# Optimization experiments

Hardware: AMD Instinct MI355X
Metric: run time of the kernel (lower is better)

Reference implementation:

```python
import jax, jax.numpy as jnp
import numpy as np

HIDDEN = 1024
GMM = 16


def setup_inputs() -> dict:
    key = jax.random.key(0)
    ks = jax.random.split(key, 9)
    B, T, D, S = 16, 1024, HIDDEN, 512
    sc_ih = 1.0 / np.sqrt(2 * D)
    sc_hh = 1.0 / np.sqrt(D)
    return {
        "input_h_c": jax.random.normal(ks[0], (B, T, D), jnp.float32),
        "memory": jax.random.normal(ks[1], (B, S, D), jnp.float32),
        "input_lengths": jax.random.randint(ks[2], (B,), 1, S + 1),
        "W_ih": jax.random.uniform(ks[3], (4 * D, 2 * D), jnp.float32, -sc_ih, sc_ih),
        "W_hh": jax.random.uniform(ks[4], (4 * D, D), jnp.float32, -sc_hh, sc_hh),
        "b_ih": jax.random.uniform(ks[5], (4 * D,), jnp.float32, -sc_hh, sc_hh),
        "b_hh": jax.random.uniform(ks[6], (4 * D,), jnp.float32, -sc_hh, sc_hh),
        "Wg_w": jax.random.uniform(ks[7], (3 * GMM, D), jnp.float32, -sc_hh, sc_hh),
        "Wg_b": jax.random.uniform(ks[8], (3 * GMM,), jnp.float32, -sc_hh, sc_hh),
    }


def reference(input_h_c, memory, input_lengths, W_ih, W_hh, b_ih, b_hh, Wg_w, Wg_b):
    B, T, D = input_h_c.shape
    S = memory.shape[1]
    M = Wg_b.shape[0] // 3
    b = b_ih + b_hh
    u = jnp.arange(S, dtype=input_h_c.dtype)  # positions u

    def step(carry, x_t):
        h, c, ctx = carry
        x = jnp.concatenate([x_t, ctx], axis=-1)  # [B, 2D]
        gates = x @ W_ih.T + h @ W_hh.T + b  # [B, 4D], torch gate order i,f,g,o
        i_g, f_g, g_g, o_g = jnp.split(gates, 4, axis=-1)
        c = jax.nn.sigmoid(f_g) * c + jax.nn.sigmoid(i_g) * jnp.tanh(g_g)
        h = jax.nn.sigmoid(o_g) * jnp.tanh(c)
        phi = h @ Wg_w.T + Wg_b  # [B, 3M]
        ksi = jnp.exp(phi[:, :M])
        beta = jnp.exp(phi[:, M:2 * M])
        alpha = jax.nn.softmax(phi[:, 2 * M:], axis=-1)
        # 1/(1+exp((ksi-u)/beta)) == sigmoid((u-ksi)/beta)
        z = (u[None, None, :] - ksi[:, :, None]) / beta[:, :, None]  # [B,M,S]
        half = 0.5 / beta[:, :, None]
        F_R = jax.nn.sigmoid(z + half)  # CDF at u+0.5
        F_L = jax.nn.sigmoid(z - half)  # CDF at u-0.5
        w = jnp.einsum('bm,bms->bs', alpha, F_R - F_L)  # [B,S]
        term = 1.0 - jnp.einsum('bm,bms->bs', alpha, F_R)  # [B,S]
        ctx = jnp.einsum('bs,bsd->bd', w, memory)  # [B,D]
        return (h, c, ctx), (w, term)

    h0 = jnp.zeros((B, D), input_h_c.dtype)
    c0 = jnp.zeros((B, D), input_h_c.dtype)
    ctx0 = jnp.zeros((B, D), input_h_c.dtype)
    (h, c, ctx), (ws, terms) = jax.lax.scan(
        step, (h0, c0, ctx0), jnp.swapaxes(input_h_c, 0, 1))
    alignment = jnp.swapaxes(ws, 0, 1)  # [B,T,S]
    term_last = terms[-1]  # [B,S]
    termination = jnp.take_along_axis(term_last, (input_lengths - 1)[:, None], axis=1)  # [B,1]
    context = ctx[:, None, :]  # [B,1,D], last-step context (as returned by torch forward)
    return (context, alignment, termination)
```

## Files before the change

kernel.cpp:

```cpp
#include <hip/hip_runtime.h>
#include <hip/hip_fp16.h>

#define BB 16
#define TT 1024
#define DD 1024
#define SS 512
#define KK2 2048

#define NBLK 128
#define NTHR 512

#define OUT_ALIGN 16384
#define OUT_TERM  8404992

typedef __attribute__((ext_vector_type(8))) short short8;
typedef __attribute__((ext_vector_type(4))) float floatx4;
typedef __attribute__((ext_vector_type(2))) _Float16 half2v;

struct KParams {
  const float* x;
  const float* mem;
  const int*   lens;
  const float* W_ih;
  const float* W_hh;
  const float* b_ih;
  const float* b_hh;
  const float* Wg_w;
  const float* Wg_b;
  float* out;
  unsigned* bar;
  unsigned short* xc0;
  unsigned short* xc1;
  unsigned* wgbf;
};

__device__ __forceinline__ float sigf(float v) {
  return __builtin_amdgcn_rcpf(1.0f + __expf(-v));
}
__device__ __forceinline__ float tanhfast(float v) {
  float a = fabsf(v);
  float e = __expf(-2.0f * a);
  float r = (1.0f - e) * __builtin_amdgcn_rcpf(1.0f + e);
  return v < 0.0f ? -r : r;
}

__device__ __forceinline__ unsigned short f2bf(float f) {
  unsigned u = __float_as_uint(f);
  return (unsigned short)((u + 0x7FFFu + ((u >> 16) & 1u)) >> 16);
}
__device__ __forceinline__ float bf2f(unsigned short h) {
  return __uint_as_float(((unsigned)h) << 16);
}
__device__ __forceinline__ unsigned pack2bf(float a, float b) {
  return (unsigned)f2bf(a) | ((unsigned)f2bf(b) << 16);
}
__device__ __forceinline__ unsigned cvtpk(float a, float b) {
  unsigned r;
  asm volatile("v_cvt_pk_bf16_f32 %0, %1, %2" : "=v"(r) : "v"(a), "v"(b));
  return r;
}

__device__ __forceinline__ void cstore_u32(unsigned* p2, unsigned v) {
  __hip_atomic_store(p2, v, __ATOMIC_RELAXED, __HIP_MEMORY_SCOPE_AGENT);
}
__device__ __forceinline__ unsigned cload_u32(const unsigned* p2) {
  return __hip_atomic_load(p2, __ATOMIC_RELAXED, __HIP_MEMORY_SCOPE_AGENT);
}
__device__ __forceinline__ unsigned long long cload_u64(const unsigned long long* p2) {
  return __hip_atomic_load(p2, __ATOMIC_RELAXED, __HIP_MEMORY_SCOPE_AGENT);
}

__device__ __forceinline__ void lds_barrier() {
  asm volatile("s_waitcnt lgkmcnt(0)\n\ts_barrier" ::: "memory");
}

__device__ __forceinline__ void grid_barrier(unsigned* bar, unsigned ep, int blk) {
  __syncthreads();
  if (threadIdx.x == 0) cstore_u32(&bar[64 + blk * 32], ep);
  if (threadIdx.x < 64) {
    while (cload_u32(&bar[64 + (int)threadIdx.x * 32]) < ep) __builtin_amdgcn_s_sleep(1);
    while (cload_u32(&bar[64 + ((int)threadIdx.x + 64) * 32]) < ep) __builtin_amdgcn_s_sleep(1);
  }
  __syncthreads();
}

union UF { unsigned w[4]; unsigned long long u[2]; short8 s; };

#define MFMA16 __builtin_amdgcn_mfma_f32_16x16x32_bf16

__device__ __forceinline__ void xh_mfma(const UF* xf, const UF* hf, const short8* bfr,
                                        floatx4& a00, floatx4& a01,
                                        floatx4& a10, floatx4& a11) {
  floatx4 z = {0.f, 0.f, 0.f, 0.f};
  a00 = z; a01 = z; a10 = z; a11 = z;
  a00 = MFMA16(xf[0].s, bfr[0],  a00, 0, 0, 0); a01 = MFMA16(xf[1].s, bfr[1],  a01, 0, 0, 0);
  a10 = MFMA16(xf[0].s, bfr[12], a10, 0, 0, 0); a11 = MFMA16(xf[1].s, bfr[13], a11, 0, 0, 0);
  a00 = MFMA16(xf[2].s, bfr[2],  a00, 0, 0, 0); a01 = MFMA16(xf[3].s, bfr[3],  a01, 0, 0, 0);
  a10 = MFMA16(xf[2].s, bfr[14], a10, 0, 0, 0); a11 = MFMA16(xf[3].s, bfr[15], a11, 0, 0, 0);
  a00 = MFMA16(hf[0].s, bfr[8],  a00, 0, 0, 0); a01 = MFMA16(hf[1].s, bfr[9],  a01, 0, 0, 0);
  a10 = MFMA16(hf[0].s, bfr[20], a10, 0, 0, 0); a11 = MFMA16(hf[1].s, bfr[21], a11, 0, 0, 0);
  a00 = MFMA16(hf[2].s, bfr[10], a00, 0, 0, 0); a01 = MFMA16(hf[3].s, bfr[11], a01, 0, 0, 0);
  a10 = MFMA16(hf[2].s, bfr[22], a10, 0, 0, 0); a11 = MFMA16(hf[3].s, bfr[23], a11, 0, 0, 0);
}

__global__ __launch_bounds__(NTHR, 2) void tts_kernel(KParams p) {
  extern __shared__ char smem[];
  half2v* memsh2 = (half2v*)smem;

  __shared__ float redC[64 * 65 + 4];
  __shared__ unsigned hshu[8 * 65];
  __shared__ float php[384];
  __shared__ float alsh[16], ksish[16], invbsh[16];
  __shared__ float Rsh[513];
  __shared__ half2v wsh2[256];
  __shared__ float ctxp[4][128];
  __shared__ float bsh48[48];

  const int t    = threadIdx.x;
  const int blk  = blockIdx.x;
  const int lane = t & 63;
  const int w    = t >> 6;
  const int bbt  = blk & 15;
  const int dc   = blk >> 4;

  short8 bfr[24];
  {
    const int n = lane & 15;
    const int q = lane >> 4;
#pragma unroll
    for (int nt = 0; nt < 2; ++nt) {
      const int r = (n & 3) * 1024 + blk * 8 + nt * 4 + (n >> 2);
#pragma unroll
      for (int ki = 0; ki < 12; ++ki) {
        short8 v;
        const int k0 = (ki >> 2) * 1024 + w * 128 + (ki & 3) * 32 + q * 8;
#pragma unroll
        for (int j = 0; j < 8; ++j) {
          int k = k0 + j;
          float wv = (k < 2048) ? p.W_ih[(size_t)r * 2048 + k]
                                : p.W_hh[(size_t)r * 1024 + (k - 2048)];
          v[j] = (short)f2bf(wv);
        }
        bfr[nt * 12 + ki] = v;
      }
    }
  }
  float biasreg[4] = {0.f, 0.f, 0.f, 0.f};
  if (t < 128) {
    int dl = t & 7;
#pragma unroll
    for (int g = 0; g < 4; ++g) {
      int r = g * 1024 + blk * 8 + dl;
      biasreg[g] = p.b_ih[r] + p.b_hh[r];
    }
  }
  if (t < 48) bsh48[t] = p.Wg_b[t];
  {
    int dl = t & 127, sp = t >> 7;
    for (int pr = sp; pr < 256; pr += 4) {
      const float* mp = p.mem + (size_t)bbt * SS * DD + (size_t)(2 * pr) * DD + dc * 128 + dl;
      half2v v;
      v.x = (_Float16)mp[0];
      v.y = (_Float16)mp[DD];
      memsh2[pr * 128 + dl] = v;
    }
  }
  if (blk == 0) {
    for (int i = t; i < 48 * 512; i += NTHR)
      cstore_u32(&p.wgbf[i], pack2bf(p.Wg_w[2 * i], p.Wg_w[2 * i + 1]));
  }
  grid_barrier(p.bar, 1u, blk);

  float c_val = 0.0f;
  unsigned ep = 1;
  unsigned short* xc_cur = p.xc0;
  unsigned short* xc_nxt = p.xc1;
  const int ab2 = ((lane & 15) * KK2 + w * 128 + ((lane >> 4) * 8)) >> 2;
  const float* xrow = p.x + (size_t)(lane & 15) * TT * DD + w * 128 + ((lane >> 4) * 8);

  floatx4 acc00, acc01, acc10, acc11;
  {
    UF xf[4], hf[4];
#pragma unroll
    for (int sub = 0; sub < 4; ++sub) {
      floatx4 lo = *(const floatx4*)(xrow + sub * 32);
      floatx4 hi = *(const floatx4*)(xrow + sub * 32 + 4);
      xf[sub].w[0] = cvtpk(lo[0], lo[1]); xf[sub].w[1] = cvtpk(lo[2], lo[3]);
      xf[sub].w[2] = cvtpk(hi[0], hi[1]); xf[sub].w[3] = cvtpk(hi[2], hi[3]);
    }
    const unsigned long long* hb = (const unsigned long long*)p.xc0 + ab2 + 256;
#pragma unroll
    for (int sub = 0; sub < 4; ++sub) {
      hf[sub].u[0] = cload_u64(hb + sub * 8);
      hf[sub].u[1] = cload_u64(hb + sub * 8 + 1);
    }
    xh_mfma(xf, hf, bfr, acc00, acc01, acc10, acc11);
  }

  for (int tstep = 0; tstep < TT; ++tstep) {
    {
      const unsigned long long* cb = (const unsigned long long*)xc_cur + ab2;
      UF fc[4];
#pragma unroll
      for (int sub = 0; sub < 4; ++sub) {
        fc[sub].u[0] = cload_u64(cb + sub * 8);
        fc[sub].u[1] = cload_u64(cb + sub * 8 + 1);
      }
      floatx4 c00 = acc00, c01 = acc01, c10 = acc10, c11 = acc11;
      c00 = MFMA16(fc[0].s, bfr[4],  c00, 0, 0, 0); c01 = MFMA16(fc[1].s, bfr[5],  c01, 0, 0, 0);
      c10 = MFMA16(fc[0].s, bfr[16], c10, 0, 0, 0); c11 = MFMA16(fc[1].s, bfr[17], c11, 0, 0, 0);
      c00 = MFMA16(fc[2].s, bfr[6],  c00, 0, 0, 0); c01 = MFMA16(fc[3].s, bfr[7],  c01, 0, 0, 0);
      c10 = MFMA16(fc[2].s, bfr[18], c10, 0, 0, 0); c11 = MFMA16(fc[3].s, bfr[19], c11, 0, 0, 0);
      c00 += c01; c10 += c11;
#pragma unroll
      for (int reg = 0; reg < 4; ++reg) {
        redC[(w * 8 + reg) * 65 + lane]     = c00[reg];
        redC[(w * 8 + 4 + reg) * 65 + lane] = c10[reg];
      }
    }
    lds_barrier();
    if (t < 128) {
      int b = t >> 3, dl = t & 7, nt = dl >> 2, dl4 = dl & 3;
      int row = nt * 4 + (b & 3);
      float gate[4];
#pragma unroll
      for (int g = 0; g < 4; ++g) {
        int ls = ((b >> 2) << 4) | (dl4 * 4 + g);
        float s = biasreg[g];
#pragma unroll
        for (int w2 = 0; w2 < 8; ++w2) s += redC[(w2 * 8 + row) * 65 + ls];
        gate[g] = s;
      }
      c_val = sigf(gate[1]) * c_val + sigf(gate[0]) * tanhfast(gate[2]);
      float hv = sigf(gate[3]) * tanhfast(c_val);
      float hn = __shfl_down(hv, 1, 64);
      if ((t & 1) == 0)
        cstore_u32((unsigned*)(xc_nxt + b * KK2 + 1024 + blk * 8 + dl), pack2bf(hv, hn));
    }
    grid_barrier(p.bar, ++ep, blk);

    unsigned long long hword = 0;
    if (t < 256) hword = cload_u64((const unsigned long long*)xc_nxt + bbt * 512 + 256 + t);
    UF hf[4];
    floatx4 xlo[4], xhi[4];
    if (tstep + 1 < TT) {
      const unsigned long long* hb = (const unsigned long long*)xc_nxt + ab2 + 256;
#pragma unroll
      for (int sub = 0; sub < 4; ++sub) {
        hf[sub].u[0] = cload_u64(hb + sub * 8);
        hf[sub].u[1] = cload_u64(hb + sub * 8 + 1);
      }
      const float* xp = xrow + (size_t)(tstep + 1) * DD;
#pragma unroll
      for (int sub = 0; sub < 4; ++sub) {
        xlo[sub] = *(const floatx4*)(xp + sub * 32);
        xhi[sub] = *(const floatx4*)(xp + sub * 32 + 4);
      }
    }
    if (t < 256) {
      int row = t >> 5, col = (t & 31) * 2;
      hshu[row * 65 + col]     = (unsigned)hword;
      hshu[row * 65 + col + 1] = (unsigned)(hword >> 32);
    }
    lds_barrier();
    if (t < 384) {
      int m = t >> 3, part = t & 7;
      const unsigned* wgp = p.wgbf + m * 512 + part * 64;
      const unsigned* hrow = hshu + part * 65;
      float s0 = 0.f, s1 = 0.f, s2 = 0.f, s3 = 0.f;
#pragma unroll 4
      for (int i = 0; i < 64; i += 4) {
        unsigned u0 = hrow[i],     g0 = wgp[i];
        unsigned u1 = hrow[i + 1], g1 = wgp[i + 1];
        unsigned u2 = hrow[i + 2], g2 = wgp[i + 2];
        unsigned u3 = hrow[i + 3], g3 = wgp[i + 3];
        s0 += bf2f((unsigned short)u0) * bf2f((unsigned short)g0)
            + bf2f((unsigned short)(u0 >> 16)) * bf2f((unsigned short)(g0 >> 16));
        s1 += bf2f((unsigned short)u1) * bf2f((unsigned short)g1)
            + bf2f((unsigned short)(u1 >> 16)) * bf2f((unsigned short)(g1 >> 16));
        s2 += bf2f((unsigned short)u2) * bf2f((unsigned short)g2)
            + bf2f((unsigned short)(u2 >> 16)) * bf2f((unsigned short)(g2 >> 16));
        s3 += bf2f((unsigned short)u3) * bf2f((unsigned short)g3)
            + bf2f((unsigned short)(u3 >> 16)) * bf2f((unsigned short)(g3 >> 16));
      }
      php[t] = (s0 + s1) + (s2 + s3);
    }
    lds_barrier();
    if (t < 64) {
      float s = 0.f;
      if (t < 48) {
        s = bsh48[t];
#pragma unroll
        for (int i = 0; i < 8; ++i) s += php[t * 8 + i];
      }
      float mx = s;
#pragma unroll
      for (int o = 1; o < 16; o <<= 1) mx = fmaxf(mx, __shfl_xor(mx, o, 64));
      float e = __expf(s - mx);
      float sm = e;
#pragma unroll
      for (int o = 1; o < 16; o <<= 1) sm += __shfl_xor(sm, o, 64);
      float alpha_v = e * __builtin_amdgcn_rcpf(sm);
      float ksi_v   = __expf(s);
      float invb_v  = __expf(-s);
      if (t >= 32) { if (t < 48) alsh[t - 32] = alpha_v; }
      else if (t < 16) ksish[t] = ksi_v;
      else invbsh[t - 16] = invb_v;
      int m = t & 15;
      float am = __shfl(alpha_v, 32 + m, 64);
      float km = __shfl(ksi_v, m, 64);
      float bm = __shfl(invb_v, 16 + m, 64);
      float term = am * sigf((-0.5f - km) * bm);
#pragma unroll
      for (int o = 1; o < 16; o <<= 1) term += __shfl_xor(term, o, 64);
      if (t == 48) Rsh[0] = term;
    }
    lds_barrier();
    {
      float su = (float)t;
      float rv0 = 0.f, rv1 = 0.f;
#pragma unroll
      for (int m = 0; m < 16; m += 2) {
        rv0 += alsh[m]     * sigf((su + 0.5f - ksish[m])     * invbsh[m]);
        rv1 += alsh[m + 1] * sigf((su + 0.5f - ksish[m + 1]) * invbsh[m + 1]);
      }
      float rv = rv0 + rv1;
      float rvp = __shfl_up(rv, 1, 64);
      float rvn = __shfl_down(rv, 1, 64);
      Rsh[t + 1] = rv;
      if ((t & 1) == 0) {
        half2v v2;
        v2.x = (_Float16)(rv - rvp);
        v2.y = (_Float16)(rvn - rv);
        wsh2[t >> 1] = v2;
      }
      if (dc == 0 && (t & 63) != 0)
        p.out[OUT_ALIGN + ((size_t)bbt * TT + tstep) * SS + t] = rv - rvp;
    }
    lds_barrier();
    {
      if (dc == 0 && t < 8)
        p.out[OUT_ALIGN + ((size_t)bbt * TT + tstep) * SS + 64 * t] =
            Rsh[64 * t + 1] - Rsh[64 * t];
      if (tstep == TT - 1 && dc == 0 && t == 0)
        p.out[OUT_TERM + bbt] = 1.0f - Rsh[p.lens[bbt]];
      int dl = t & 127, sp = t >> 7;
      const int pb = sp * 64;
      half2v wa = wsh2[pb];       wa.x = (_Float16)(Rsh[2 * pb + 1] - Rsh[2 * pb]);
      half2v wb = wsh2[pb + 32];  wb.x = (_Float16)(Rsh[2 * pb + 65] - Rsh[2 * pb + 64]);
      float s0 = __builtin_amdgcn_fdot2(memsh2[pb * 128 + dl], wa, 0.f, false);
      float s1 = __builtin_amdgcn_fdot2(memsh2[(pb + 32) * 128 + dl], wb, 0.f, false);
#pragma unroll 8
      for (int q = 1; q < 32; ++q) {
        s0 = __builtin_amdgcn_fdot2(memsh2[(pb + q) * 128 + dl],      wsh2[pb + q],      s0, false);
        s1 = __builtin_amdgcn_fdot2(memsh2[(pb + 32 + q) * 128 + dl], wsh2[pb + 32 + q], s1, false);
      }
      ctxp[sp][dl] = s0 + s1;
    }
    lds_barrier();
    if (t < 128) {
      float cv = ctxp[0][t] + ctxp[1][t] + ctxp[2][t] + ctxp[3][t];
      if (tstep == TT - 1) p.out[bbt * DD + dc * 128 + t] = cv;
      float cvn = __shfl_down(cv, 1, 64);
      if ((t & 1) == 0)
        cstore_u32((unsigned*)(xc_nxt + bbt * KK2 + dc * 128 + t), pack2bf(cv, cvn));
    }
    __builtin_amdgcn_sched_barrier(0);
    if (tstep + 1 < TT) {
      UF xf[4];
#pragma unroll
      for (int sub = 0; sub < 4; ++sub) {
        xf[sub].w[0] = cvtpk(xlo[sub][0], xlo[sub][1]);
        xf[sub].w[1] = cvtpk(xlo[sub][2], xlo[sub][3]);
        xf[sub].w[2] = cvtpk(xhi[sub][0], xhi[sub][1]);
        xf[sub].w[3] = cvtpk(xhi[sub][2], xhi[sub][3]);
      }
      xh_mfma(xf, hf, bfr, acc00, acc01, acc10, acc11);
    }
    grid_barrier(p.bar, ++ep, blk);

    unsigned short* tmp = xc_cur; xc_cur = xc_nxt; xc_nxt = tmp;
  }
}

extern "C" void kernel_launch(void* const* d_in, const int* in_sizes, int n_in,
                              void* d_out, int out_size, void* d_ws, size_t ws_size,
                              hipStream_t stream) {
  (void)in_sizes; (void)n_in; (void)out_size; (void)ws_size;
  KParams p;
  p.x    = (const float*)d_in[0];
  p.mem  = (const float*)d_in[1];
  p.lens = (const int*)d_in[2];
  p.W_ih = (const float*)d_in[3];
  p.W_hh = (const float*)d_in[4];
  p.b_ih = (const float*)d_in[5];
  p.b_hh = (const float*)d_in[6];
  p.Wg_w = (const float*)d_in[7];
  p.Wg_b = (const float*)d_in[8];
  p.out  = (float*)d_out;
  p.bar  = (unsigned*)d_ws;
  p.xc0  = (unsigned short*)((char*)d_ws + 36864);
  p.xc1  = (unsigned short*)((char*)d_ws + 36864 + 65536);
  p.wgbf = (unsigned*)((char*)d_ws + 36864 + 131072);

  hipMemsetAsync(d_ws, 0, 36864 + 65536, stream);

  const unsigned dynLds = 131072;
  hipFuncSetAttribute((const void*)tts_kernel, hipFuncAttributeMaxDynamicSharedMemorySize,
                      (int)dynLds);

  void* args[] = { &p };
  hipLaunchCooperativeKernel((const void*)tts_kernel, dim3(NBLK), dim3(NTHR), args, dynLds,
                             stream);
}
```

Measured before the change: 16.19 ms.

## Compute attention phi projection with MFMA from register-resident Wg weights

Replaces the scalar bf16 dot-product phi projection (h @ Wg_w^T), which staged h through LDS and read a global bf16 copy of Wg, with MFMA instructions. These use Wg fragments preloaded into registers and the h fragments already loaded for the LSTM step. The setup grid barrier and global Wg staging are removed, and the grid barrier polling is simplified to one load per thread across 128 threads. The x-to-bf16 conversion is moved earlier. The aim is to shorten the serial per-timestep critical path, at the cost of 12 extra short8 registers per thread and redundant phi work across batch lanes.

```diff
diff --git a/kernel.cpp b/kernel.cpp
--- a/kernel.cpp
+++ b/kernel.cpp
@@ -31,7 +31,6 @@
   unsigned* bar;
   unsigned short* xc0;
   unsigned short* xc1;
-  unsigned* wgbf;
 };
 
 __device__ __forceinline__ float sigf(float v) {
@@ -48,9 +47,6 @@
   unsigned u = __float_as_uint(f);
   return (unsigned short)((u + 0x7FFFu + ((u >> 16) & 1u)) >> 16);
 }
-__device__ __forceinline__ float bf2f(unsigned short h) {
-  return __uint_as_float(((unsigned)h) << 16);
-}
 __device__ __forceinline__ unsigned pack2bf(float a, float b) {
   return (unsigned)f2bf(a) | ((unsigned)f2bf(b) << 16);
 }
@@ -77,9 +73,8 @@
 __device__ __forceinline__ void grid_barrier(unsigned* bar, unsigned ep, int blk) {
   __syncthreads();
   if (threadIdx.x == 0) cstore_u32(&bar[64 + blk * 32], ep);
-  if (threadIdx.x < 64) {
+  if (threadIdx.x < NBLK) {
     while (cload_u32(&bar[64 + (int)threadIdx.x * 32]) < ep) __builtin_amdgcn_s_sleep(1);
-    while (cload_u32(&bar[64 + ((int)threadIdx.x + 64) * 32]) < ep) __builtin_amdgcn_s_sleep(1);
   }
   __syncthreads();
 }
@@ -103,13 +98,16 @@
   a10 = MFMA16(hf[2].s, bfr[22], a10, 0, 0, 0); a11 = MFMA16(hf[3].s, bfr[23], a11, 0, 0, 0);
 }
 
+__device__ __forceinline__ float sel4(const floatx4& v, int r) {
+  return (r == 0) ? v[0] : (r == 1) ? v[1] : (r == 2) ? v[2] : v[3];
+}
+
 __global__ __launch_bounds__(NTHR, 2) void tts_kernel(KParams p) {
   extern __shared__ char smem[];
   half2v* memsh2 = (half2v*)smem;
 
   __shared__ float redC[64 * 65 + 4];
-  __shared__ unsigned hshu[8 * 65];
-  __shared__ float php[384];
+  __shared__ float phiP[384];
   __shared__ float alsh[16], ksish[16], invbsh[16];
   __shared__ float Rsh[513];
   __shared__ half2v wsh2[256];
@@ -144,6 +142,21 @@
         bfr[nt * 12 + ki] = v;
       }
     }
+  }
+  short8 wgB[12];
+  {
+    const int n = lane & 15;
+    const int q = lane >> 4;
+#pragma unroll
+    for (int tau = 0; tau < 3; ++tau)
+#pragma unroll
+      for (int c = 0; c < 4; ++c) {
+        short8 v;
+        const float* wg = p.Wg_w + (size_t)(tau * 16 + n) * 1024 + w * 128 + c * 32 + q * 8;
+#pragma unroll
+        for (int j = 0; j < 8; ++j) v[j] = (short)f2bf(wg[j]);
+        wgB[tau * 4 + c] = v;
+      }
   }
   float biasreg[4] = {0.f, 0.f, 0.f, 0.f};
   if (t < 128) {
@@ -165,14 +178,9 @@
       memsh2[pr * 128 + dl] = v;
     }
   }
-  if (blk == 0) {
-    for (int i = t; i < 48 * 512; i += NTHR)
-      cstore_u32(&p.wgbf[i], pack2bf(p.Wg_w[2 * i], p.Wg_w[2 * i + 1]));
-  }
-  grid_barrier(p.bar, 1u, blk);
 
   float c_val = 0.0f;
-  unsigned ep = 1;
+  unsigned ep = 0;
   unsigned short* xc_cur = p.xc0;
   unsigned short* xc_nxt = p.xc1;
   const int ab2 = ((lane & 15) * KK2 + w * 128 + ((lane >> 4) * 8)) >> 2;
@@ -239,51 +247,47 @@
     }
     grid_barrier(p.bar, ++ep, blk);
 
-    unsigned long long hword = 0;
-    if (t < 256) hword = cload_u64((const unsigned long long*)xc_nxt + bbt * 512 + 256 + t);
     UF hf[4];
-    floatx4 xlo[4], xhi[4];
-    if (tstep + 1 < TT) {
+    {
       const unsigned long long* hb = (const unsigned long long*)xc_nxt + ab2 + 256;
 #pragma unroll
       for (int sub = 0; sub < 4; ++sub) {
         hf[sub].u[0] = cload_u64(hb + sub * 8);
         hf[sub].u[1] = cload_u64(hb + sub * 8 + 1);
       }
+    }
+    UF xf[4];
+    if (tstep + 1 < TT) {
       const float* xp = xrow + (size_t)(tstep + 1) * DD;
 #pragma unroll
       for (int sub = 0; sub < 4; ++sub) {
-        xlo[sub] = *(const floatx4*)(xp + sub * 32);
-        xhi[sub] = *(const floatx4*)(xp + sub * 32 + 4);
-      }
-    }
-    if (t < 256) {
-      int row = t >> 5, col = (t & 31) * 2;
-      hshu[row * 65 + col]     = (unsigned)hword;
-      hshu[row * 65 + col + 1] = (unsigned)(hword >> 32);
-    }
-    lds_barrier();
-    if (t < 384) {
-      int m = t >> 3, part = t & 7;
-      const unsigned* wgp = p.wgbf + m * 512 + part * 64;
-      const unsigned* hrow = hshu + part * 65;
-      float s0 = 0.f, s1 = 0.f, s2 = 0.f, s3 = 0.f;
-#pragma unroll 4
-      for (int i = 0; i < 64; i += 4) {
-        unsigned u0 = hrow[i],     g0 = wgp[i];
-        unsigned u1 = hrow[i + 1], g1 = wgp[i + 1];
-        unsigned u2 = hrow[i + 2], g2 = wgp[i + 2];
-        unsigned u3 = hrow[i + 3], g3 = wgp[i + 3];
-        s0 += bf2f((unsigned short)u0) * bf2f((unsigned short)g0)
-            + bf2f((unsigned short)(u0 >> 16)) * bf2f((unsigned short)(g0 >> 16));
-        s1 += bf2f((unsigned short)u1) * bf2f((unsigned short)g1)
-            + bf2f((unsigned short)(u1 >> 16)) * bf2f((unsigned short)(g1 >> 16));
-        s2 += bf2f((unsigned short)u2) * bf2f((unsigned short)g2)
-            + bf2f((unsigned short)(u2 >> 16)) * bf2f((unsigned short)(g2 >> 16));
-        s3 += bf2f((unsigned short)u3) * bf2f((unsigned short)g3)
-            + bf2f((unsigned short)(u3 >> 16)) * bf2f((unsigned short)(g3 >> 16));
-      }
-      php[t] = (s0 + s1) + (s2 + s3);
+        floatx4 lo = *(const floatx4*)(xp + sub * 32);
+        floatx4 hi = *(const floatx4*)(xp + sub * 32 + 4);
+        xf[sub].w[0] = cvtpk(lo[0], lo[1]); xf[sub].w[1] = cvtpk(lo[2], lo[3]);
+        xf[sub].w[2] = cvtpk(hi[0], hi[1]); xf[sub].w[3] = cvtpk(hi[2], hi[3]);
+      }
+    }
+    {
+      floatx4 z = {0.f, 0.f, 0.f, 0.f};
+      floatx4 ph0 = z, ph1 = z, ph2 = z;
+      ph0 = MFMA16(hf[0].s, wgB[0], ph0, 0, 0, 0);
+      ph1 = MFMA16(hf[0].s, wgB[4], ph1, 0, 0, 0);
+      ph2 = MFMA16(hf[0].s, wgB[8], ph2, 0, 0, 0);
+      ph0 = MFMA16(hf[1].s, wgB[1], ph0, 0, 0, 0);
+      ph1 = MFMA16(hf[1].s, wgB[5], ph1, 0, 0, 0);
+      ph2 = MFMA16(hf[1].s, wgB[9], ph2, 0, 0, 0);
+      ph0 = MFMA16(hf[2].s, wgB[2], ph0, 0, 0, 0);
+      ph1 = MFMA16(hf[2].s, wgB[6], ph1, 0, 0, 0);
+      ph2 = MFMA16(hf[2].s, wgB[10], ph2, 0, 0, 0);
+      ph0 = MFMA16(hf[3].s, wgB[3], ph0, 0, 0, 0);
+      ph1 = MFMA16(hf[3].s, wgB[7], ph1, 0, 0, 0);
+      ph2 = MFMA16(hf[3].s, wgB[11], ph2, 0, 0, 0);
+      if ((lane >> 4) == (bbt >> 2)) {
+        int m = lane & 15, r = bbt & 3;
+        phiP[w * 48 + m]      = sel4(ph0, r);
+        phiP[w * 48 + 16 + m] = sel4(ph1, r);
+        phiP[w * 48 + 32 + m] = sel4(ph2, r);
+      }
     }
     lds_barrier();
     if (t < 64) {
@@ -291,7 +295,7 @@
       if (t < 48) {
         s = bsh48[t];
 #pragma unroll
-        for (int i = 0; i < 8; ++i) s += php[t * 8 + i];
+        for (int i = 0; i < 8; ++i) s += phiP[i * 48 + t];
       }
       float mx = s;
 #pragma unroll
@@ -367,14 +371,6 @@
     }
     __builtin_amdgcn_sched_barrier(0);
     if (tstep + 1 < TT) {
-      UF xf[4];
-#pragma unroll
-      for (int sub = 0; sub < 4; ++sub) {
-        xf[sub].w[0] = cvtpk(xlo[sub][0], xlo[sub][1]);
-        xf[sub].w[1] = cvtpk(xlo[sub][2], xlo[sub][3]);
-        xf[sub].w[2] = cvtpk(xhi[sub][0], xhi[sub][1]);
-        xf[sub].w[3] = cvtpk(xhi[sub][2], xhi[sub][3]);
-      }
       xh_mfma(xf, hf, bfr, acc00, acc01, acc10, acc11);
     }
     grid_barrier(p.bar, ++ep, blk);
@@ -401,7 +397,6 @@
   p.bar  = (unsigned*)d_ws;
   p.xc0  = (unsigned short*)((char*)d_ws + 36864);
   p.xc1  = (unsigned short*)((char*)d_ws + 36864 + 65536);
-  p.wgbf = (unsigned*)((char*)d_ws + 36864 + 131072);
 
   hipMemsetAsync(d_ws, 0, 36864 + 65536, stream);
 
```

New measurement: 13.33 ms. 17.6% less time.
